# Performance work log

Measured on AMD Instinct MI355X. Metric: run time of the kernel, lower is better.

The kernel has to match this reference:

```python
import jax, jax.numpy as jnp
import numpy as np

B, S, ENC, DEC, EMB, V = 256, 128, 512, 512, 256, 32000


def setup_inputs() -> dict:
    key = jax.random.key(0)
    ks = jax.random.split(key, 12)
    inp = {}
    inp["input_tok"] = jax.random.randint(ks[0], (B,), 0, V)
    inp["hidden"] = jax.random.normal(ks[1], (1, B, DEC), dtype=jnp.float32)
    inp["encoder_outputs"] = jax.random.normal(ks[2], (S, B, ENC), dtype=jnp.float32)
    # learned params
    inp["emb_table"] = jax.random.normal(ks[3], (V, EMB), dtype=jnp.float32) * 0.02
    inp["attn_W"] = jax.random.normal(ks[4], (ENC + DEC, DEC), dtype=jnp.float32) * 0.02
    inp["attn_b"] = jnp.zeros((DEC,), dtype=jnp.float32)
    inp["v"] = jax.random.uniform(ks[5], (DEC,), dtype=jnp.float32)
    inp["W_ih"] = jax.random.normal(ks[6], (3 * DEC, ENC + EMB), dtype=jnp.float32) * 0.02
    inp["W_hh"] = jax.random.normal(ks[7], (3 * DEC, DEC), dtype=jnp.float32) * 0.02
    inp["b_ih"] = jnp.zeros((3 * DEC,), dtype=jnp.float32)
    inp["b_hh"] = jnp.zeros((3 * DEC,), dtype=jnp.float32)
    inp["fc_W"] = jax.random.normal(ks[8], (V, ENC + DEC + EMB), dtype=jnp.float32) * 0.02
    inp["fc_b"] = jnp.zeros((V,), dtype=jnp.float32)
    return inp


def reference(input_tok, hidden, encoder_outputs, emb_table, attn_W, attn_b, v,
              W_ih, W_hh, b_ih, b_hh, fc_W, fc_b):
    # dropout is identity in eval mode
    emb = emb_table[input_tok]                      # [B, EMB]
    h = hidden[0]                                   # [B, DEC]
    s_len = encoder_outputs.shape[0]
    # Bahdanau attention: energy over [src_len, B]
    h_rep = jnp.broadcast_to(h[None], (s_len,) + h.shape)        # [S,B,DEC]
    cat = jnp.concatenate([h_rep, encoder_outputs], axis=-1)     # [S,B,ENC+DEC]
    energy = jnp.tanh(cat @ attn_W + attn_b)                     # [S,B,DEC]
    scores = jnp.einsum('sbd,d->bs', energy, v)                  # [B,S]
    a = jax.nn.softmax(scores, axis=1)                           # [B,S]
    weighted = jnp.einsum('bs,sbe->be', a, encoder_outputs)      # [B,ENC]
    # single-step GRU (PyTorch gate order: r, z, n)
    x = jnp.concatenate([emb, weighted], axis=1)                 # [B,EMB+ENC]
    gi = x @ W_ih.T + b_ih                                       # [B,3*DEC]
    gh = h @ W_hh.T + b_hh
    ir, iz, in_ = jnp.split(gi, 3, axis=1)
    hr, hz, hn = jnp.split(gh, 3, axis=1)
    r = jax.nn.sigmoid(ir + hr)
    z = jax.nn.sigmoid(iz + hz)
    n = jnp.tanh(in_ + r * hn)
    h_new = (1.0 - z) * n + z * h                                # [B,DEC]
    # output projection
    pred = jnp.concatenate([h_new, weighted, emb], axis=1) @ fc_W.T + fc_b  # [B,V]
    return pred, h_new
```

## Files before the change

### kernel.cpp

```cpp
#include <hip/hip_runtime.h>
#include <cmath>

static constexpr int B   = 256;
static constexpr int S   = 128;
static constexpr int ENC = 512;
static constexpr int DEC = 512;
static constexpr int EMB = 256;
static constexpr int V   = 32000;
static constexpr int KX  = EMB + ENC;
static constexpr int KF  = DEC + ENC + EMB;
static constexpr int G3  = 3 * DEC;

typedef __attribute__((ext_vector_type(8))) short short8v;
typedef __attribute__((ext_vector_type(4))) float f32x4;

__device__ __forceinline__ float sigmoidf(float xv) { return 1.0f / (1.0f + expf(-xv)); }

__device__ __forceinline__ unsigned short f2bf(float f) {
    unsigned u = __float_as_uint(f);
    unsigned r = (u + 0x7fffu + ((u >> 16) & 1u)) >> 16;
    return (unsigned short)r;
}
__device__ __forceinline__ float bf2f(unsigned short s) {
    return __uint_as_float(((unsigned)s) << 16);
}

template<int TRANSB, int BIAS>
__global__ __launch_bounds__(256) void gemm_f32(
    const float* __restrict__ A, const float* __restrict__ Bm,
    const float* __restrict__ bias, float* __restrict__ C,
    int M, int N, int K, int lda, int ldb, int ldc)
{
    __shared__ float As[16][68];
    __shared__ float Bs[16][68];
    const int tid  = threadIdx.x;
    const int row0 = blockIdx.y * 64;
    const int col0 = blockIdx.x * 64;
    const int tx = tid & 15, ty = tid >> 4;

    float acc[4][4] = {};
    for (int k0 = 0; k0 < K; k0 += 16) {
        {
            const int m  = tid >> 2;
            const int kk = (tid & 3) << 2;
            const float4 a4 = *reinterpret_cast<const float4*>(
                &A[(size_t)(row0 + m) * lda + k0 + kk]);
            As[kk + 0][m] = a4.x; As[kk + 1][m] = a4.y;
            As[kk + 2][m] = a4.z; As[kk + 3][m] = a4.w;
        }
        if (TRANSB) {
            const int n  = tid >> 2;
            const int kk = (tid & 3) << 2;
            const float4 b4 = *reinterpret_cast<const float4*>(
                &Bm[(size_t)(col0 + n) * ldb + k0 + kk]);
            Bs[kk + 0][n] = b4.x; Bs[kk + 1][n] = b4.y;
            Bs[kk + 2][n] = b4.z; Bs[kk + 3][n] = b4.w;
        } else {
            const int kk = tid >> 4;
            const int n  = (tid & 15) << 2;
            *reinterpret_cast<float4*>(&Bs[kk][n]) =
                *reinterpret_cast<const float4*>(&Bm[(size_t)(k0 + kk) * ldb + col0 + n]);
        }
        __syncthreads();
        #pragma unroll
        for (int k = 0; k < 16; ++k) {
            float a4[4], b4[4];
            *reinterpret_cast<float4*>(a4) = *reinterpret_cast<const float4*>(&As[k][ty << 2]);
            *reinterpret_cast<float4*>(b4) = *reinterpret_cast<const float4*>(&Bs[k][tx << 2]);
            #pragma unroll
            for (int i = 0; i < 4; ++i)
                #pragma unroll
                for (int j = 0; j < 4; ++j)
                    acc[i][j] = fmaf(a4[i], b4[j], acc[i][j]);
        }
        __syncthreads();
    }
    #pragma unroll
    for (int i = 0; i < 4; ++i) {
        const int r = row0 + (ty << 2) + i;
        #pragma unroll
        for (int j = 0; j < 4; ++j) {
            const int c = col0 + (tx << 2) + j;
            float outv = acc[i][j];
            if (BIAS) outv += bias[c];
            C[(size_t)r * ldc + c] = outv;
        }
    }
}

__global__ __launch_bounds__(256) void conv_enc(
    const float* __restrict__ src, unsigned short* __restrict__ dst)
{
    size_t base = ((size_t)blockIdx.x * 256 + threadIdx.x) * 8;
    const size_t stride = (size_t)2048 * 256 * 8;
    #pragma unroll
    for (int it = 0; it < 4; ++it, base += stride) {
        const float4 f0 = *reinterpret_cast<const float4*>(&src[base]);
        const float4 f1 = *reinterpret_cast<const float4*>(&src[base + 4]);
        short8v t;
        t[0] = (short)f2bf(f0.x); t[1] = (short)f2bf(f0.y);
        t[2] = (short)f2bf(f0.z); t[3] = (short)f2bf(f0.w);
        t[4] = (short)f2bf(f1.x); t[5] = (short)f2bf(f1.y);
        t[6] = (short)f2bf(f1.z); t[7] = (short)f2bf(f1.w);
        *reinterpret_cast<short8v*>(&dst[base]) = t;
    }
}

__global__ __launch_bounds__(256) void conv_h(
    const float* __restrict__ src, unsigned short* __restrict__ dst)
{
    const size_t base = ((size_t)blockIdx.x * 256 + threadIdx.x) * 8;
    const float4 f0 = *reinterpret_cast<const float4*>(&src[base]);
    const float4 f1 = *reinterpret_cast<const float4*>(&src[base + 4]);
    short8v t;
    t[0] = (short)f2bf(f0.x); t[1] = (short)f2bf(f0.y);
    t[2] = (short)f2bf(f0.z); t[3] = (short)f2bf(f0.w);
    t[4] = (short)f2bf(f1.x); t[5] = (short)f2bf(f1.y);
    t[6] = (short)f2bf(f1.z); t[7] = (short)f2bf(f1.w);
    *reinterpret_cast<short8v*>(&dst[base]) = t;
}

__global__ __launch_bounds__(256) void transpose_We(
    const float* __restrict__ attn_W, unsigned short* __restrict__ WeT)
{
    __shared__ float t[32][33];
    const int k0 = blockIdx.x * 32, n0 = blockIdx.y * 32;
    const int r = threadIdx.x >> 3, c4 = (threadIdx.x & 7) * 4;
    const float4 f = *reinterpret_cast<const float4*>(
        &attn_W[(size_t)(DEC + k0 + r) * DEC + n0 + c4]);
    t[r][c4] = f.x; t[r][c4 + 1] = f.y; t[r][c4 + 2] = f.z; t[r][c4 + 3] = f.w;
    __syncthreads();
    unsigned short o[4] = { f2bf(t[c4 + 0][r]), f2bf(t[c4 + 1][r]),
                            f2bf(t[c4 + 2][r]), f2bf(t[c4 + 3][r]) };
    *reinterpret_cast<uint2*>(&WeT[(size_t)(n0 + r) * 512 + k0 + c4]) =
        *reinterpret_cast<uint2*>(o);
}

__global__ __launch_bounds__(512, 4) void energy_mfma(
    const unsigned short* __restrict__ encb, const unsigned short* __restrict__ WeT,
    const float* __restrict__ hWb, const float* __restrict__ vvec,
    float* __restrict__ scores)
{
    __shared__ unsigned short Ae[128 * 72];
    __shared__ unsigned short Be[256 * 72];
    const int bid = blockIdx.x;
    const int logical = (bid & 7) * 64 + (bid >> 3);
    const int mb = logical >> 1, nb = logical & 1;
    const int tid = threadIdx.x, lane = tid & 63, wid = tid >> 6;
    const int wm = wid >> 2, wn = wid & 3;
    const int l15 = lane & 15, lk = lane >> 4;

    f32x4 acc[4][4] = {};
    for (int k0 = 0; k0 < 512; k0 += 64) {
        #pragma unroll
        for (int j = 0; j < 2; ++j) {
            const int ci = tid + 512 * j;
            const int row = ci >> 3, kc = ci & 7;
            *reinterpret_cast<short8v*>(&Ae[row * 72 + kc * 8]) =
                *reinterpret_cast<const short8v*>(
                    &encb[(size_t)(mb * 128 + row) * 512 + k0 + kc * 8]);
        }
        #pragma unroll
        for (int j = 0; j < 4; ++j) {
            const int ci = tid + 512 * j;
            const int row = ci >> 3, kc = ci & 7;
            *reinterpret_cast<short8v*>(&Be[row * 72 + kc * 8]) =
                *reinterpret_cast<const short8v*>(
                    &WeT[(size_t)(nb * 256 + row) * 512 + k0 + kc * 8]);
        }
        __syncthreads();
        #pragma unroll
        for (int kk = 0; kk < 2; ++kk) {
            short8v bfr[4];
            #pragma unroll
            for (int nf = 0; nf < 4; ++nf)
                bfr[nf] = *reinterpret_cast<const short8v*>(
                    &Be[(wn * 64 + nf * 16 + l15) * 72 + kk * 32 + lk * 8]);
            #pragma unroll
            for (int mf = 0; mf < 4; ++mf) {
                const short8v afr = *reinterpret_cast<const short8v*>(
                    &Ae[(wm * 64 + mf * 16 + l15) * 72 + kk * 32 + lk * 8]);
                #pragma unroll
                for (int nf = 0; nf < 4; ++nf)
                    acc[mf][nf] = __builtin_amdgcn_mfma_f32_16x16x32_bf16(
                        afr, bfr[nf], acc[mf][nf], 0, 0, 0);
            }
        }
        __syncthreads();
    }
    const int colbase = nb * 256 + wn * 64;
    #pragma unroll
    for (int mf = 0; mf < 4; ++mf) {
        #pragma unroll
        for (int r = 0; r < 4; ++r) {
            const int rl = wm * 64 + mf * 16 + lk * 4 + r;
            const int g  = mb * 128 + rl;
            const int b  = g & (B - 1);
            float p = 0.0f;
            #pragma unroll
            for (int nf = 0; nf < 4; ++nf) {
                const int col = colbase + nf * 16 + l15;
                p += vvec[col] * tanhf(acc[mf][nf][r] + hWb[(size_t)b * DEC + col]);
            }
            p += __shfl_xor(p, 1, 64);
            p += __shfl_xor(p, 2, 64);
            p += __shfl_xor(p, 4, 64);
            p += __shfl_xor(p, 8, 64);
            if (l15 == 0) atomicAdd(&scores[g], p);
        }
    }
}

__global__ __launch_bounds__(512) void fc_mfma(
    const unsigned short* __restrict__ xcatb, const float* __restrict__ fcW,
    const float* __restrict__ fcb, float* __restrict__ pred)
{
    __shared__ unsigned short As[256 * 72];
    __shared__ unsigned short Bs[64 * 72];
    const int n0 = blockIdx.x * 64;
    const int tid = threadIdx.x, lane = tid & 63, wid = tid >> 6;
    const int wm = wid >> 1, wn = wid & 1;
    const int l15 = lane & 15, lk = lane >> 4;

    f32x4 acc[4][2] = {};
    for (int k0 = 0; k0 < KF; k0 += 64) {
        #pragma unroll
        for (int j = 0; j < 4; ++j) {
            const int ci = tid + 512 * j;
            const int row = ci >> 3, kc = ci & 7;
            *reinterpret_cast<short8v*>(&As[row * 72 + kc * 8]) =
                *reinterpret_cast<const short8v*>(
                    &xcatb[(size_t)row * KF + k0 + kc * 8]);
        }
        {
            const int row = tid >> 3, kc = tid & 7;
            const float* src = &fcW[(size_t)(n0 + row) * KF + k0 + kc * 8];
            const float4 f0 = *reinterpret_cast<const float4*>(src);
            const float4 f1 = *reinterpret_cast<const float4*>(src + 4);
            short8v t;
            t[0] = (short)f2bf(f0.x); t[1] = (short)f2bf(f0.y);
            t[2] = (short)f2bf(f0.z); t[3] = (short)f2bf(f0.w);
            t[4] = (short)f2bf(f1.x); t[5] = (short)f2bf(f1.y);
            t[6] = (short)f2bf(f1.z); t[7] = (short)f2bf(f1.w);
            *reinterpret_cast<short8v*>(&Bs[row * 72 + kc * 8]) = t;
        }
        __syncthreads();
        #pragma unroll
        for (int kk = 0; kk < 2; ++kk) {
            short8v bfr[2];
            #pragma unroll
            for (int nf = 0; nf < 2; ++nf)
                bfr[nf] = *reinterpret_cast<const short8v*>(
                    &Bs[(wn * 32 + nf * 16 + l15) * 72 + kk * 32 + lk * 8]);
            #pragma unroll
            for (int mf = 0; mf < 4; ++mf) {
                const short8v afr = *reinterpret_cast<const short8v*>(
                    &As[(wm * 64 + mf * 16 + l15) * 72 + kk * 32 + lk * 8]);
                acc[mf][0] = __builtin_amdgcn_mfma_f32_16x16x32_bf16(
                    afr, bfr[0], acc[mf][0], 0, 0, 0);
                acc[mf][1] = __builtin_amdgcn_mfma_f32_16x16x32_bf16(
                    afr, bfr[1], acc[mf][1], 0, 0, 0);
            }
        }
        __syncthreads();
    }
    #pragma unroll
    for (int mf = 0; mf < 4; ++mf) {
        const int grow0 = wm * 64 + mf * 16 + lk * 4;
        #pragma unroll
        for (int nf = 0; nf < 2; ++nf) {
            const int gcol = n0 + wn * 32 + nf * 16 + l15;
            const float bias = fcb[gcol];
            #pragma unroll
            for (int r = 0; r < 4; ++r)
                pred[(size_t)(grow0 + r) * V + gcol] = acc[mf][nf][r] + bias;
        }
    }
}

__global__ __launch_bounds__(256) void gemm_bf16_small(
    const unsigned short* __restrict__ Abf, const float* __restrict__ Wf,
    const float* __restrict__ bias, float* __restrict__ C, int K, int ldc)
{
    __shared__ unsigned short As[256 * 72];
    __shared__ unsigned short Bs[64 * 72];
    const int n0 = blockIdx.x * 64;
    const int tid = threadIdx.x, lane = tid & 63, wid = tid >> 6;
    const int wm = wid >> 1, wn = wid & 1;
    const int l15 = lane & 15, lk = lane >> 4;

    f32x4 acc[8][2] = {};
    for (int k0 = 0; k0 < K; k0 += 64) {
        #pragma unroll
        for (int j = 0; j < 8; ++j) {
            const int ci = tid + 256 * j;
            const int row = ci >> 3, kc = ci & 7;
            *reinterpret_cast<short8v*>(&As[row * 72 + kc * 8]) =
                *reinterpret_cast<const short8v*>(
                    &Abf[(size_t)row * K + k0 + kc * 8]);
        }
        #pragma unroll
        for (int j = 0; j < 2; ++j) {
            const int ci = tid + 256 * j;
            const int row = ci >> 3, kc = ci & 7;
            const float* src = &Wf[(size_t)(n0 + row) * K + k0 + kc * 8];
            const float4 f0 = *reinterpret_cast<const float4*>(src);
            const float4 f1 = *reinterpret_cast<const float4*>(src + 4);
            short8v t;
            t[0] = (short)f2bf(f0.x); t[1] = (short)f2bf(f0.y);
            t[2] = (short)f2bf(f0.z); t[3] = (short)f2bf(f0.w);
            t[4] = (short)f2bf(f1.x); t[5] = (short)f2bf(f1.y);
            t[6] = (short)f2bf(f1.z); t[7] = (short)f2bf(f1.w);
            *reinterpret_cast<short8v*>(&Bs[row * 72 + kc * 8]) = t;
        }
        __syncthreads();
        #pragma unroll
        for (int kk = 0; kk < 2; ++kk) {
            short8v bfr[2];
            #pragma unroll
            for (int nf = 0; nf < 2; ++nf)
                bfr[nf] = *reinterpret_cast<const short8v*>(
                    &Bs[(wn * 32 + nf * 16 + l15) * 72 + kk * 32 + lk * 8]);
            #pragma unroll
            for (int mf = 0; mf < 8; ++mf) {
                const short8v afr = *reinterpret_cast<const short8v*>(
                    &As[(wm * 128 + mf * 16 + l15) * 72 + kk * 32 + lk * 8]);
                acc[mf][0] = __builtin_amdgcn_mfma_f32_16x16x32_bf16(
                    afr, bfr[0], acc[mf][0], 0, 0, 0);
                acc[mf][1] = __builtin_amdgcn_mfma_f32_16x16x32_bf16(
                    afr, bfr[1], acc[mf][1], 0, 0, 0);
            }
        }
        __syncthreads();
    }
    #pragma unroll
    for (int mf = 0; mf < 8; ++mf) {
        const int grow0 = wm * 128 + mf * 16 + lk * 4;
        #pragma unroll
        for (int nf = 0; nf < 2; ++nf) {
            const int gcol = n0 + wn * 32 + nf * 16 + l15;
            const float bv = bias[gcol];
            #pragma unroll
            for (int r = 0; r < 4; ++r)
                C[(size_t)(grow0 + r) * ldc + gcol] = acc[mf][nf][r] + bv;
        }
    }
}

__global__ __launch_bounds__(256) void softmax_weighted(
    const float* __restrict__ scores, const unsigned short* __restrict__ encb,
    unsigned short* __restrict__ xcatb, unsigned short* __restrict__ xb)
{
    const int b   = blockIdx.x;
    const int tid = threadIdx.x;
    __shared__ float sa[S];
    __shared__ float red[128];

    const float sc = (tid < S) ? scores[(size_t)tid * B + b] : -1e30f;
    if (tid < 128) red[tid] = sc;
    __syncthreads();
    for (int off = 64; off >= 1; off >>= 1) {
        if (tid < off) red[tid] = fmaxf(red[tid], red[tid + off]);
        __syncthreads();
    }
    const float mx = red[0];
    __syncthreads();
    const float e = (tid < S) ? expf(sc - mx) : 0.0f;
    if (tid < 128) red[tid] = e;
    __syncthreads();
    for (int off = 64; off >= 1; off >>= 1) {
        if (tid < off) red[tid] += red[tid + off];
        __syncthreads();
    }
    const float inv = 1.0f / red[0];
    __syncthreads();
    if (tid < S) sa[tid] = e * inv;
    __syncthreads();

    float acc0 = 0.0f, acc1 = 0.0f;
    const int e0 = tid * 2;
    for (int s = 0; s < S; ++s) {
        const float w = sa[s];
        const unsigned u = *reinterpret_cast<const unsigned*>(
            &encb[((size_t)s * B + b) * ENC + e0]);
        acc0 = fmaf(w, bf2f((unsigned short)(u & 0xffffu)), acc0);
        acc1 = fmaf(w, bf2f((unsigned short)(u >> 16)), acc1);
    }
    unsigned short t2[2] = { f2bf(acc0), f2bf(acc1) };
    const unsigned packed = *reinterpret_cast<unsigned*>(t2);
    *reinterpret_cast<unsigned*>(&xcatb[(size_t)b * KF + DEC + e0]) = packed;
    *reinterpret_cast<unsigned*>(&xb[(size_t)b * KX + EMB + e0])    = packed;
}

__global__ void gather_emb(const int* __restrict__ tok, const float* __restrict__ table,
                           unsigned short* __restrict__ xcatb, unsigned short* __restrict__ xb)
{
    const int b = blockIdx.x, t = threadIdx.x;
    const float4 v4 = *reinterpret_cast<const float4*>(
        &table[(size_t)tok[b] * EMB + t * 4]);
    unsigned short o[4] = { f2bf(v4.x), f2bf(v4.y), f2bf(v4.z), f2bf(v4.w) };
    const uint2 p = *reinterpret_cast<uint2*>(o);
    *reinterpret_cast<uint2*>(&xcatb[(size_t)b * KF + DEC + ENC + t * 4]) = p;
    *reinterpret_cast<uint2*>(&xb[(size_t)b * KX + t * 4]) = p;
}

__global__ __launch_bounds__(256) void gru_gates(
    const float* __restrict__ gi, const float* __restrict__ gh,
    const float* __restrict__ h, unsigned short* __restrict__ xcatb,
    float* __restrict__ h_out)
{
    const int idx = blockIdx.x * 256 + threadIdx.x;
    const int b = idx >> 9, d = idx & 511;
    const float* gib = gi + (size_t)b * G3;
    const float* ghb = gh + (size_t)b * G3;
    const float r  = sigmoidf(gib[d] + ghb[d]);
    const float z  = sigmoidf(gib[DEC + d] + ghb[DEC + d]);
    const float n  = tanhf(gib[2 * DEC + d] + r * ghb[2 * DEC + d]);
    const float hv = h[(size_t)b * DEC + d];
    const float hn = (1.0f - z) * n + z * hv;
    xcatb[(size_t)b * KF + d] = f2bf(hn);
    h_out[(size_t)b * DEC + d] = hn;
}

extern "C" void kernel_launch(void* const* d_in, const int* in_sizes, int n_in,
                              void* d_out, int out_size, void* d_ws, size_t ws_size,
                              hipStream_t stream)
{
    const int*   tok    = (const int*)d_in[0];
    const float* hidden = (const float*)d_in[1];
    const float* enc    = (const float*)d_in[2];
    const float* table  = (const float*)d_in[3];
    const float* attn_W = (const float*)d_in[4];
    const float* attn_b = (const float*)d_in[5];
    const float* vvec   = (const float*)d_in[6];
    const float* W_ih   = (const float*)d_in[7];
    const float* W_hh   = (const float*)d_in[8];
    const float* b_ih   = (const float*)d_in[9];
    const float* b_hh   = (const float*)d_in[10];
    const float* fc_W   = (const float*)d_in[11];
    const float* fc_b   = (const float*)d_in[12];

    float* ws     = (float*)d_ws;
    float* hWb    = ws;
    float* scores = hWb + B * DEC;
    float* gi     = scores + S * B;
    float* gh     = gi + B * G3;
    unsigned short* xcatb = (unsigned short*)(gh + B * G3);
    unsigned short* WeT   = xcatb + (size_t)B * KF;
    unsigned short* xb    = WeT + (size_t)512 * 512;
    unsigned short* hb    = xb + (size_t)B * KX;
    unsigned short* encb  = hb + (size_t)B * DEC;

    float* pred  = (float*)d_out;
    float* h_out = pred + (size_t)B * V;

    hipMemsetAsync(scores, 0, (size_t)S * B * sizeof(float), stream);

    conv_enc<<<2048, 256, 0, stream>>>(enc, encb);
    conv_h<<<64, 256, 0, stream>>>(hidden, hb);
    transpose_We<<<dim3(16, 16), 256, 0, stream>>>(attn_W, WeT);
    gather_emb<<<B, 64, 0, stream>>>(tok, table, xcatb, xb);

    gemm_f32<0, 1><<<dim3(DEC / 64, B / 64), 256, 0, stream>>>(
        hidden, attn_W, attn_b, hWb, B, DEC, DEC, DEC, DEC, DEC);

    energy_mfma<<<512, 512, 0, stream>>>(encb, WeT, hWb, vvec, scores);

    softmax_weighted<<<B, 256, 0, stream>>>(scores, encb, xcatb, xb);

    gemm_bf16_small<<<G3 / 64, 256, 0, stream>>>(xb, W_ih, b_ih, gi, KX, G3);
    gemm_bf16_small<<<G3 / 64, 256, 0, stream>>>(hb, W_hh, b_hh, gh, DEC, G3);

    gru_gates<<<(B * DEC) / 256, 256, 0, stream>>>(gi, gh, hidden, xcatb, h_out);

    fc_mfma<<<V / 64, 512, 0, stream>>>(xcatb, fc_W, fc_b, pred);
}
```

Baseline: 477.3 us.

## Register-prefetch FC GEMM tiles and merge the two GRU GEMM launches

```diff
diff --git a/kernel.cpp b/kernel.cpp
--- a/kernel.cpp
+++ b/kernel.cpp
@@ -221,28 +221,53 @@
     const int tid = threadIdx.x, lane = tid & 63, wid = tid >> 6;
     const int wm = wid >> 1, wn = wid & 1;
     const int l15 = lane & 15, lk = lane >> 4;
+    const int brow = tid >> 3, bkc = tid & 7;
+
+    short8v aReg[4];
+    float4  bR0, bR1;
+
+    #pragma unroll
+    for (int j = 0; j < 4; ++j) {
+        const int ci = tid + 512 * j;
+        const int row = ci >> 3, kc = ci & 7;
+        aReg[j] = *reinterpret_cast<const short8v*>(
+            &xcatb[(size_t)row * KF + kc * 8]);
+    }
+    {
+        const float* src = &fcW[(size_t)(n0 + brow) * KF + bkc * 8];
+        bR0 = *reinterpret_cast<const float4*>(src);
+        bR1 = *reinterpret_cast<const float4*>(src + 4);
+    }
 
     f32x4 acc[4][2] = {};
-    for (int k0 = 0; k0 < KF; k0 += 64) {
+    for (int t = 0; t < KF / 64; ++t) {
+        __syncthreads();
         #pragma unroll
         for (int j = 0; j < 4; ++j) {
             const int ci = tid + 512 * j;
             const int row = ci >> 3, kc = ci & 7;
-            *reinterpret_cast<short8v*>(&As[row * 72 + kc * 8]) =
-                *reinterpret_cast<const short8v*>(
+            *reinterpret_cast<short8v*>(&As[row * 72 + kc * 8]) = aReg[j];
+        }
+        {
+            short8v tB;
+            tB[0] = (short)f2bf(bR0.x); tB[1] = (short)f2bf(bR0.y);
+            tB[2] = (short)f2bf(bR0.z); tB[3] = (short)f2bf(bR0.w);
+            tB[4] = (short)f2bf(bR1.x); tB[5] = (short)f2bf(bR1.y);
+            tB[6] = (short)f2bf(bR1.z); tB[7] = (short)f2bf(bR1.w);
+            *reinterpret_cast<short8v*>(&Bs[brow * 72 + bkc * 8]) = tB;
+        }
+        if (t + 1 < KF / 64) {
+            const int k0 = (t + 1) * 64;
+            #pragma unroll
+            for (int j = 0; j < 4; ++j) {
+                const int ci = tid + 512 * j;
+                const int row = ci >> 3, kc = ci & 7;
+                aReg[j] = *reinterpret_cast<const short8v*>(
                     &xcatb[(size_t)row * KF + k0 + kc * 8]);
-        }
-        {
-            const int row = tid >> 3, kc = tid & 7;
-            const float* src = &fcW[(size_t)(n0 + row) * KF + k0 + kc * 8];
-            const float4 f0 = *reinterpret_cast<const float4*>(src);
-            const float4 f1 = *reinterpret_cast<const float4*>(src + 4);
-            short8v t;
-            t[0] = (short)f2bf(f0.x); t[1] = (short)f2bf(f0.y);
-            t[2] = (short)f2bf(f0.z); t[3] = (short)f2bf(f0.w);
-            t[4] = (short)f2bf(f1.x); t[5] = (short)f2bf(f1.y);
-            t[6] = (short)f2bf(f1.z); t[7] = (short)f2bf(f1.w);
-            *reinterpret_cast<short8v*>(&Bs[row * 72 + kc * 8]) = t;
+            }
+            const float* src = &fcW[(size_t)(n0 + brow) * KF + k0 + bkc * 8];
+            bR0 = *reinterpret_cast<const float4*>(src);
+            bR1 = *reinterpret_cast<const float4*>(src + 4);
         }
         __syncthreads();
         #pragma unroll
@@ -262,7 +287,6 @@
                     afr, bfr[1], acc[mf][1], 0, 0, 0);
             }
         }
-        __syncthreads();
     }
     #pragma unroll
     for (int mf = 0; mf < 4; ++mf) {
@@ -278,13 +302,22 @@
     }
 }
 
-__global__ __launch_bounds__(256) void gemm_bf16_small(
-    const unsigned short* __restrict__ Abf, const float* __restrict__ Wf,
-    const float* __restrict__ bias, float* __restrict__ C, int K, int ldc)
-{
+__global__ __launch_bounds__(256) void gru_gemms(
+    const unsigned short* __restrict__ xb, const float* __restrict__ W_ih,
+    const float* __restrict__ b_ih, float* __restrict__ gi,
+    const unsigned short* __restrict__ hb, const float* __restrict__ W_hh,
+    const float* __restrict__ b_hh, float* __restrict__ gh)
+{
+    const bool second = blockIdx.x >= (G3 / 64);
+    const unsigned short* Abf = second ? hb : xb;
+    const float* Wf   = second ? W_hh : W_ih;
+    const float* bias = second ? b_hh : b_ih;
+    float* C          = second ? gh : gi;
+    const int K       = second ? DEC : KX;
+    const int n0 = (second ? blockIdx.x - G3 / 64 : blockIdx.x) * 64;
+
     __shared__ unsigned short As[256 * 72];
     __shared__ unsigned short Bs[64 * 72];
-    const int n0 = blockIdx.x * 64;
     const int tid = threadIdx.x, lane = tid & 63, wid = tid >> 6;
     const int wm = wid >> 1, wn = wid & 1;
     const int l15 = lane & 15, lk = lane >> 4;
@@ -342,7 +375,7 @@
             const float bv = bias[gcol];
             #pragma unroll
             for (int r = 0; r < 4; ++r)
-                C[(size_t)(grow0 + r) * ldc + gcol] = acc[mf][nf][r] + bv;
+                C[(size_t)(grow0 + r) * G3 + gcol] = acc[mf][nf][r] + bv;
         }
     }
 }
@@ -379,6 +412,7 @@
 
     float acc0 = 0.0f, acc1 = 0.0f;
     const int e0 = tid * 2;
+    #pragma unroll 8
     for (int s = 0; s < S; ++s) {
         const float w = sa[s];
         const unsigned u = *reinterpret_cast<const unsigned*>(
@@ -468,8 +502,8 @@
 
     softmax_weighted<<<B, 256, 0, stream>>>(scores, encb, xcatb, xb);
 
-    gemm_bf16_small<<<G3 / 64, 256, 0, stream>>>(xb, W_ih, b_ih, gi, KX, G3);
-    gemm_bf16_small<<<G3 / 64, 256, 0, stream>>>(hb, W_hh, b_hh, gh, DEC, G3);
+    gru_gemms<<<2 * (G3 / 64), 256, 0, stream>>>(xb, W_ih, b_ih, gi,
+                                                 hb, W_hh, b_hh, gh);
 
     gru_gates<<<(B * DEC) / 256, 256, 0, stream>>>(gi, gh, hidden, xcatb, h_out);
 
```

Result: faster. 456.6 us (-4.3%).
